# Kernel optimization log

Hardware: AMD Instinct MI355X
Metric: run time of the kernel (lower is better)

Reference implementation:

```python
import jax, jax.numpy as jnp
import numpy as np
from jax.scipy.linalg import solve_triangular

# Production config from MFAWrapper.from_path: 28x28 images, 50 components, 6 factors
B, DFT, K, L = 2048, 784, 50, 6
LOG2PI = float(np.log(2.0 * np.pi))


def setup_inputs() -> dict:
    key = jax.random.key(0)
    k1, k2, k3, k4, k5, k6 = jax.random.split(key, 6)
    X = jax.random.normal(k1, (B, DFT), dtype=jnp.float32)
    J = jax.random.randint(k2, (B, DFT), 0, 2).astype(jnp.int32)  # binary observation mask
    MU = jax.random.normal(k3, (K, DFT), dtype=jnp.float32) * 0.5
    A_fac = jax.random.normal(k4, (K, DFT, L), dtype=jnp.float32) * 0.1  # factor loadings
    log_D = jax.random.normal(k5, (K, DFT), dtype=jnp.float32) * 0.1 - 1.0  # log noise variances
    PI_logits = jax.random.normal(k6, (K,), dtype=jnp.float32)
    return {"X": X, "J": J, "MU": MU, "A_fac": A_fac, "log_D": log_D, "PI_logits": PI_logits}


def _mfa_conditional(X, J, MU, A_fac, log_D, PI_logits):
    """Batched MFA conditional reconstruction given observed features (mask J==1).

    The per-sample torch.nonzero selection is replaced by mask-weighted linear
    algebra: restricting to observed rows of diag(1/D) is identical to zeroing
    the unobserved entries of the weight, so all B samples are conditioned in
    one batched pass instead of a Python loop.
    """
    dtype = X.dtype
    l = A_fac.shape[-1]
    Jf = (J == 1).astype(dtype)                 # [B, Dft]
    inv_D = jnp.exp(-log_D)                     # [K, Dft]
    # masked residual per (sample, component): [B, K, Dft]
    md = (X[:, None, :] - MU[None, :, :]) * Jf[:, None, :]
    # latent posterior precision P = I + A_o^T D_o^{-1} A_o  -> [B, K, L, L]
    P = jnp.einsum('bd,kd,kdi,kdj->bkij', Jf, inv_D, A_fac, A_fac) + jnp.eye(l, dtype=dtype)
    # q = A_o^T D_o^{-1} (x_o - mu_o)  -> [B, K, L]
    q = jnp.einsum('bkd,kd,kdi->bki', md, inv_D, A_fac)
    # per-component log-likelihood of observed features via Woodbury / matrix det lemma
    Lc = jnp.linalg.cholesky(P)                                         # [B, K, L, L]
    y = solve_triangular(Lc, q[..., None], lower=True)[..., 0]          # [B, K, L]
    quad = jnp.einsum('bkd,kd->bk', md * md, inv_D) - jnp.sum(y * y, axis=-1)
    logdet = (2.0 * jnp.sum(jnp.log(jnp.diagonal(Lc, axis1=-2, axis2=-1)), axis=-1)
              + jnp.einsum('bd,kd->bk', Jf, log_D))
    n_obs = jnp.sum(Jf, axis=-1, keepdims=True)                         # [B, 1]
    log_lik = -0.5 * (quad + logdet + n_obs * LOG2PI)                   # [B, K]
    log_resp = jax.nn.log_softmax(PI_logits)[None, :] + log_lik
    c = jnp.argmax(log_resp, axis=-1)                                   # most responsible component, [B]
    # gather per-sample selected component and form the conditional Gaussian in factor form
    P_sel = jnp.take_along_axis(P, c[:, None, None, None], axis=1)[:, 0]  # [B, L, L]
    q_sel = jnp.take_along_axis(q, c[:, None, None], axis=1)[:, 0]        # [B, L]
    A_sel = A_fac[c]                                                      # [B, Dft, L]
    m_z = jnp.linalg.solve(P_sel, q_sel[..., None])[..., 0]               # posterior latent mean [B, L]
    cov_z = jnp.linalg.inv(P_sel)                                         # posterior latent cov [B, L, L]
    Lz = jnp.linalg.cholesky(cov_z)
    M = MU[c] + jnp.einsum('bdi,bi->bd', A_sel, m_z)                      # conditional mean over all features
    A_out = jnp.einsum('bdi,bij->bdj', A_sel, Lz)                         # loadings: cond cov = A_out A_out^T + diag(D_out)
    D_out = jnp.exp(log_D)[c]                                             # [B, Dft]
    Pw = jnp.ones((X.shape[0], 1), dtype)
    return Pw, M, A_out, D_out


def reference(X, J, MU, A_fac, log_D, PI_logits):
    return _mfa_conditional(X, J, MU, A_fac, log_D, PI_logits)
```

## Files before the change

### kernel.cpp

```cpp
#include <hip/hip_runtime.h>
#include <math.h>

#define B_N 2048
#define D_FT 784
#define K_N 50
#define L_N 6
#define LOG2PI_F 1.8378770664093453f

#define OUT_PW 0
#define OUT_M  (B_N)
#define OUT_A  (OUT_M + B_N*D_FT)
#define OUT_D  (OUT_A + B_N*D_FT*6)

#define WS_SCORES 0
#define WS_PQ     (WS_SCORES + K_N*B_N)
#define WS_C      (WS_PQ + K_N*27*B_N)
#define WS_MZLZ   (WS_C + B_N)
#define WS_XT     (WS_MZLZ + B_N*28)
#define WS_JBT    (WS_XT + D_FT*B_N)

#define IDX(i,j) ((i)*((i)+1)/2 + (j))

typedef float v2f __attribute__((ext_vector_type(2)));

#define PK_FMA(acc, a, b) asm("v_pk_fma_f32 %0, %1, %2, %0" : "+v"(acc) : "v"(a), "v"(b))

__device__ __forceinline__ void chol6(const float* P, float* L, float* rd, float* sumlog) {
    float sl = 0.f;
    #pragma unroll
    for (int j = 0; j < 6; ++j) {
        float s = P[IDX(j,j)];
        #pragma unroll
        for (int m = 0; m < j; ++m) s -= L[IDX(j,m)] * L[IDX(j,m)];
        float d = sqrtf(s);
        L[IDX(j,j)] = d;
        float r = 1.0f / d;
        rd[j] = r;
        sl += logf(d);
        #pragma unroll
        for (int i = j + 1; i < 6; ++i) {
            float t = P[IDX(i,j)];
            #pragma unroll
            for (int m = 0; m < j; ++m) t -= L[IDX(i,m)] * L[IDX(j,m)];
            L[IDX(i,j)] = t * r;
        }
    }
    *sumlog = sl;
}

__global__ __launch_bounds__(1024) void k_prep(const float* __restrict__ X,
                                               const int* __restrict__ J,
                                               float4* __restrict__ Xt4,
                                               unsigned* __restrict__ JbT) {
    const int bid = blockIdx.x;
    const int tid = threadIdx.x;
    if (bid < 448) {
        __shared__ float4 tile[32][33];
        int tx = tid & 31, ty = tid >> 5;
        int d4b = (bid % 7) * 32;
        int bb  = (bid / 7) * 32;
        int d4 = d4b + tx;
        if (d4 < D_FT / 4)
            tile[ty][tx] = *(const float4*)&X[(size_t)(bb + ty) * D_FT + d4 * 4];
        __syncthreads();
        int d4o = d4b + ty;
        if (d4o < D_FT / 4)
            Xt4[(size_t)d4o * B_N + (bb + tx)] = tile[tx][ty];
    } else {
        int t = (bid - 448) * 1024 + tid;
        int b = t >> 5;
        int w = t & 31;
        if (w >= 25) return;
        int d0 = w * 32;
        int n = D_FT - d0; if (n > 32) n = 32;
        unsigned u = 0;
        for (int j = 0; j < n; ++j)
            u |= (J[(size_t)b * D_FT + d0 + j] != 0 ? 1u : 0u) << j;
        JbT[(size_t)w * B_N + b] = u;
    }
}

__global__ __launch_bounds__(256) void k_jld(const float* __restrict__ logD,
                                             const unsigned* __restrict__ JbT,
                                             float* __restrict__ SJL) {
    __shared__ float ld[800];
    const int k  = blockIdx.x >> 3;
    const int bt = blockIdx.x & 7;
    for (int i = threadIdx.x; i < 800; i += 256)
        ld[i] = (i < D_FT) ? logD[(size_t)k * D_FT + i] : 0.f;
    __syncthreads();
    const int b = bt * 256 + threadIdx.x;
    float jl = 0.f;
    for (int w = 0; w < 25; ++w) {
        unsigned mw = JbT[(size_t)w * B_N + b];
        const float* lw = &ld[w * 32];
        #pragma unroll
        for (int dd = 0; dd < 32; ++dd)
            jl += ((mw >> dd) & 1u) ? lw[dd] : 0.f;
    }
    SJL[(size_t)k * B_N + b] = jl;
}

#define ACC_PAIR(pi, dd, x0, x1) do { \
    const float4 f0 = sm4[(size_t)(pi) * 4 + 0]; \
    const float4 f1 = sm4[(size_t)(pi) * 4 + 1]; \
    const float4 f2 = sm4[(size_t)(pi) * 4 + 2]; \
    const float4 f3 = sm4[(size_t)(pi) * 4 + 3]; \
    v2f m2;  m2.x = (float)((mw >> (dd)) & 1u); m2.y = (float)((mw >> ((dd)+1)) & 1u); \
    v2f x2;  x2.x = (x0); x2.y = (x1); \
    v2f sa2;  sa2.x = f3.x;  sa2.y = f3.y; \
    v2f nmu2; nmu2.x = f3.z; nmu2.y = f3.w; \
    v2f xm2 = x2 + nmu2; \
    v2f w2  = m2 * sa2; \
    v2f z2  = w2 * xm2; \
    v2f a0; a0.x = f0.x; a0.y = f0.y;  v2f a1; a1.x = f0.z; a1.y = f0.w; \
    v2f a2; a2.x = f1.x; a2.y = f1.y;  v2f a3; a3.x = f1.z; a3.y = f1.w; \
    v2f a4; a4.x = f2.x; a4.y = f2.y;  v2f a5; a5.x = f2.z; a5.y = f2.w; \
    v2f u0 = m2 * a0, u1 = m2 * a1, u2 = m2 * a2; \
    v2f u3 = m2 * a3, u4 = m2 * a4, u5 = m2 * a5; \
    PK_FMA(Pm2[0],  u0, u0); \
    PK_FMA(Pm2[1],  u1, u0); PK_FMA(Pm2[2],  u1, u1); \
    PK_FMA(Pm2[3],  u2, u0); PK_FMA(Pm2[4],  u2, u1); PK_FMA(Pm2[5],  u2, u2); \
    PK_FMA(Pm2[6],  u3, u0); PK_FMA(Pm2[7],  u3, u1); PK_FMA(Pm2[8],  u3, u2); PK_FMA(Pm2[9],  u3, u3); \
    PK_FMA(Pm2[10], u4, u0); PK_FMA(Pm2[11], u4, u1); PK_FMA(Pm2[12], u4, u2); PK_FMA(Pm2[13], u4, u3); PK_FMA(Pm2[14], u4, u4); \
    PK_FMA(Pm2[15], u5, u0); PK_FMA(Pm2[16], u5, u1); PK_FMA(Pm2[17], u5, u2); PK_FMA(Pm2[18], u5, u3); PK_FMA(Pm2[19], u5, u4); PK_FMA(Pm2[20], u5, u5); \
    PK_FMA(qv2[0], z2, u0); PK_FMA(qv2[1], z2, u1); PK_FMA(qv2[2], z2, u2); \
    PK_FMA(qv2[3], z2, u3); PK_FMA(qv2[4], z2, u4); PK_FMA(qv2[5], z2, u5); \
    PK_FMA(quad2, z2, z2); \
} while (0)

__global__ __launch_bounds__(256, 4) void k_accum(
        const float4* __restrict__ Xt4, const unsigned* __restrict__ JbT,
        const float* __restrict__ A, const float* __restrict__ MU,
        const float* __restrict__ logD, const float* __restrict__ PI,
        float* __restrict__ scores, float* __restrict__ Pq) {
    __shared__ float4 sm4[200 * 4];
    float* smem = (float*)sm4;
    const int k   = blockIdx.x >> 5;
    const int tid = threadIdx.x;
    const int s   = tid & 63;
    const int h   = tid >> 6;
    const int b   = (blockIdx.x & 31) * 64 + s;

    v2f Pm2[21], qv2[6], quad2;
    #pragma unroll
    for (int t = 0; t < 21; ++t) { Pm2[t].x = 0.f; Pm2[t].y = 0.f; }
    #pragma unroll
    for (int t = 0; t < 6; ++t) { qv2[t].x = 0.f; qv2[t].y = 0.f; }
    quad2.x = 0.f; quad2.y = 0.f;
    int nob = 0;

    for (int c = 0; c < 2; ++c) {
        const int dbase = c ? 384 : 0;
        const int npair = c ? 200 : 192;
        __syncthreads();
        for (int p = tid; p < npair; p += 256) {
            const int d0 = dbase + 2 * p;
            const float* ar0 = A + ((size_t)k * D_FT + d0) * 6;
            const float* ar1 = ar0 + 6;
            float sa0 = expf(-0.5f * logD[(size_t)k * D_FT + d0]);
            float sa1 = expf(-0.5f * logD[(size_t)k * D_FT + d0 + 1]);
            float4 f0, f1, f2, f3;
            f0.x = sa0 * ar0[0]; f0.y = sa1 * ar1[0]; f0.z = sa0 * ar0[1]; f0.w = sa1 * ar1[1];
            f1.x = sa0 * ar0[2]; f1.y = sa1 * ar1[2]; f1.z = sa0 * ar0[3]; f1.w = sa1 * ar1[3];
            f2.x = sa0 * ar0[4]; f2.y = sa1 * ar1[4]; f2.z = sa0 * ar0[5]; f2.w = sa1 * ar1[5];
            f3.x = sa0; f3.y = sa1;
            f3.z = -MU[(size_t)k * D_FT + d0];
            f3.w = -MU[(size_t)k * D_FT + d0 + 1];
            sm4[(size_t)p * 4 + 0] = f0;
            sm4[(size_t)p * 4 + 1] = f1;
            sm4[(size_t)p * 4 + 2] = f2;
            sm4[(size_t)p * 4 + 3] = f3;
        }
        __syncthreads();

        const int wb = (c ? 12 : 0) + 3 * h;
        for (int w = wb; w < wb + 3; ++w) {
            const unsigned mw = JbT[(size_t)w * B_N + b];
            nob += __popc(mw);
            const int plb = w * 16 - (dbase >> 1);
            const float4* xp = Xt4 + (size_t)(w * 8) * B_N + b;
            #pragma unroll 2
            for (int g = 0; g < 8; ++g) {
                float4 xv = xp[(size_t)g * B_N];
                ACC_PAIR(plb + 2 * g,     g * 4,     xv.x, xv.y);
                ACC_PAIR(plb + 2 * g + 1, g * 4 + 2, xv.z, xv.w);
            }
        }
        if (c == 1 && h == 3) {
            const unsigned mw = JbT[(size_t)24 * B_N + b];
            nob += __popc(mw);
            const int plb = 24 * 16 - 192;
            const float4* xp = Xt4 + (size_t)(24 * 8) * B_N + b;
            #pragma unroll
            for (int g = 0; g < 4; ++g) {
                float4 xv = xp[(size_t)g * B_N];
                ACC_PAIR(plb + 2 * g,     g * 4,     xv.x, xv.y);
                ACC_PAIR(plb + 2 * g + 1, g * 4 + 2, xv.z, xv.w);
            }
        }
    }

    float Pm[21], qv[6], quad;
    #pragma unroll
    for (int t = 0; t < 21; ++t) Pm[t] = Pm2[t].x + Pm2[t].y;
    #pragma unroll
    for (int t = 0; t < 6; ++t) qv[t] = qv2[t].x + qv2[t].y;
    quad = quad2.x + quad2.y;

    __syncthreads();
    float* red = smem;
    #define SLAB_WR do { float* o = &red[s * 33]; \
        _Pragma("unroll") for (int t = 0; t < 21; ++t) o[t] = Pm[t]; \
        _Pragma("unroll") for (int t = 0; t < 6; ++t) o[21 + t] = qv[t]; \
        o[27] = quad; o[28] = (float)nob; } while (0)
    #define SLAB_ADD do { const float* o = &red[s * 33]; \
        _Pragma("unroll") for (int t = 0; t < 21; ++t) Pm[t] += o[t]; \
        _Pragma("unroll") for (int t = 0; t < 6; ++t) qv[t] += o[21 + t]; \
        quad += o[27]; nob += (int)o[28]; } while (0)

    if (h == 1) SLAB_WR;
    __syncthreads();
    if (h == 0) SLAB_ADD;
    __syncthreads();
    if (h == 3) SLAB_WR;
    __syncthreads();
    if (h == 2) SLAB_ADD;
    __syncthreads();
    if (h == 2) SLAB_WR;
    __syncthreads();
    if (h == 0) {
        SLAB_ADD;
        float nobs = (float)nob;

        float jld = scores[(size_t)k * B_N + b];

        Pm[0] += 1.f; Pm[2] += 1.f; Pm[5] += 1.f; Pm[9] += 1.f; Pm[14] += 1.f; Pm[20] += 1.f;

        float Lm[21], rd[6], sumlog;
        chol6(Pm, Lm, rd, &sumlog);
        float y[6];
        #pragma unroll
        for (int j = 0; j < 6; ++j) {
            float sv = qv[j];
            #pragma unroll
            for (int m = 0; m < j; ++m) sv -= Lm[IDX(j,m)] * y[m];
            y[j] = sv * rd[j];
        }
        float yy = 0.f;
        #pragma unroll
        for (int j = 0; j < 6; ++j) yy += y[j] * y[j];
        float logdet = 2.f * sumlog + jld;
        float ll = -0.5f * ((quad - yy) + logdet + nobs * LOG2PI_F);
        float score = ll + PI[k];

        scores[(size_t)k * B_N + b] = score;
        float* pq = Pq + (size_t)k * 27 * B_N + b;
        #pragma unroll
        for (int t = 0; t < 21; ++t) pq[(size_t)t * B_N] = Pm[t];
        #pragma unroll
        for (int t = 0; t < 6; ++t) pq[(size_t)(21 + t) * B_N] = qv[t];
    }
}

__global__ void k_select(const float* __restrict__ scores, const float* __restrict__ Pq,
                         int* __restrict__ csel, float* __restrict__ mzLz,
                         float* __restrict__ out) {
    int b = blockIdx.x * blockDim.x + threadIdx.x;
    if (b >= B_N) return;

    float best = scores[b];
    int bc = 0;
    for (int k = 1; k < K_N; ++k) {
        float s = scores[(size_t)k * B_N + b];
        if (s > best) { best = s; bc = k; }
    }
    csel[b] = bc;
    out[OUT_PW + b] = 1.0f;

    float Pm[21], qv[6];
    const float* pq = Pq + (size_t)bc * 27 * B_N + b;
    #pragma unroll
    for (int t = 0; t < 21; ++t) Pm[t] = pq[(size_t)t * B_N];
    #pragma unroll
    for (int t = 0; t < 6; ++t) qv[t] = pq[(size_t)(21 + t) * B_N];

    float Lm[21], rd[6], dummy;
    chol6(Pm, Lm, rd, &dummy);

    float y[6];
    #pragma unroll
    for (int j = 0; j < 6; ++j) {
        float s = qv[j];
        #pragma unroll
        for (int m = 0; m < j; ++m) s -= Lm[IDX(j,m)] * y[m];
        y[j] = s * rd[j];
    }
    float mz[6];
    #pragma unroll
    for (int ii = 5; ii >= 0; --ii) {
        float s = y[ii];
        #pragma unroll
        for (int j = ii + 1; j < 6; ++j) s -= Lm[IDX(j,ii)] * mz[j];
        mz[ii] = s * rd[ii];
    }
    float Li[21];
    #pragma unroll
    for (int j = 0; j < 6; ++j) {
        Li[IDX(j,j)] = rd[j];
        #pragma unroll
        for (int i = j + 1; i < 6; ++i) {
            float s = 0.f;
            #pragma unroll
            for (int m = j; m < i; ++m) s += Lm[IDX(i,m)] * Li[IDX(m,j)];
            Li[IDX(i,j)] = -s * rd[i];
        }
    }
    float cov[21];
    #pragma unroll
    for (int i = 0; i < 6; ++i) {
        #pragma unroll
        for (int j = 0; j <= i; ++j) {
            float s = 0.f;
            #pragma unroll
            for (int m = i; m < 6; ++m) s += Li[IDX(m,i)] * Li[IDX(m,j)];
            cov[IDX(i,j)] = s;
        }
    }
    float Lz[21], rd2[6];
    chol6(cov, Lz, rd2, &dummy);

    float* o = mzLz + (size_t)b * 28;
    #pragma unroll
    for (int t = 0; t < 6; ++t) o[t] = mz[t];
    #pragma unroll
    for (int t = 0; t < 21; ++t) o[6 + t] = Lz[t];
}

__global__ __launch_bounds__(256) void k_output(
        const float* __restrict__ A, const float* __restrict__ MU,
        const float* __restrict__ logD, const int* __restrict__ csel,
        const float* __restrict__ mzLz, float* __restrict__ out) {
    __shared__ float smz[6];
    __shared__ float sLz[21];
    __shared__ int sc;
    int b = blockIdx.x;
    if (threadIdx.x == 0) sc = csel[b];
    if (threadIdx.x < 27) {
        float v = mzLz[(size_t)b * 28 + threadIdx.x];
        if (threadIdx.x < 6) smz[threadIdx.x] = v;
        else sLz[threadIdx.x - 6] = v;
    }
    __syncthreads();
    int c = sc;

    for (int d = threadIdx.x; d < D_FT; d += 256) {
        const float* ar = A + ((size_t)c * D_FT + d) * 6;
        float a[6];
        #pragma unroll
        for (int i = 0; i < 6; ++i) a[i] = ar[i];
        float mu = MU[(size_t)c * D_FT + d];
        float ld = logD[(size_t)c * D_FT + d];
        float m = mu;
        #pragma unroll
        for (int i = 0; i < 6; ++i) m += a[i] * smz[i];
        out[OUT_M + (size_t)b * D_FT + d] = m;
        out[OUT_D + (size_t)b * D_FT + d] = expf(ld);
        float* ao = out + OUT_A + ((size_t)b * D_FT + d) * 6;
        #pragma unroll
        for (int j = 0; j < 6; ++j) {
            float s = 0.f;
            #pragma unroll
            for (int i = j; i < 6; ++i) s += a[i] * sLz[IDX(i,j)];
            ao[j] = s;
        }
    }
}

extern "C" void kernel_launch(void* const* d_in, const int* in_sizes, int n_in,
                              void* d_out, int out_size, void* d_ws, size_t ws_size,
                              hipStream_t stream) {
    (void)in_sizes; (void)n_in; (void)out_size; (void)ws_size;
    const float* X    = (const float*)d_in[0];
    const int*   J    = (const int*)d_in[1];
    const float* MU   = (const float*)d_in[2];
    const float* A    = (const float*)d_in[3];
    const float* logD = (const float*)d_in[4];
    const float* PI   = (const float*)d_in[5];
    float* out = (float*)d_out;
    float* ws  = (float*)d_ws;

    float*    scores = ws + WS_SCORES;
    float*    Pq     = ws + WS_PQ;
    int*      csel   = (int*)(ws + WS_C);
    float*    mzLz   = ws + WS_MZLZ;
    float4*   Xt4    = (float4*)(ws + WS_XT);
    unsigned* JbT    = (unsigned*)(ws + WS_JBT);

    k_prep<<<512, 1024, 0, stream>>>(X, J, Xt4, JbT);

    k_jld<<<K_N * 8, 256, 0, stream>>>(logD, JbT, scores);

    k_accum<<<32 * K_N, 256, 0, stream>>>(Xt4, JbT, A, MU, logD, PI, scores, Pq);

    k_select<<<B_N / 256, 256, 0, stream>>>(scores, Pq, csel, mzLz, out);

    k_output<<<B_N, 256, 0, stream>>>(A, MU, logD, csel, mzLz, out);
}
```

Baseline: 139.1 us.

## Fuse component selection into output kernel and batch X loads in accumulation

Merges k_select and k_output into one kernel. Every thread of each per-sample block redundantly runs the argmax over 50 scores plus the 6x6 Cholesky, solve and inverse, which removes one launch and the csel/mzLz round trip through global memory. The trade is duplicated scalar work and broadcast score loads in all 256 threads of each block. Separately, k_accum's inner loop now issues all 8 (or 4) float4 loads of X before accumulating, to get more memory-level parallelism at the cost of extra registers.

```diff
diff --git a/kernel.cpp b/kernel.cpp
--- a/kernel.cpp
+++ b/kernel.cpp
@@ -14,9 +14,7 @@
 
 #define WS_SCORES 0
 #define WS_PQ     (WS_SCORES + K_N*B_N)
-#define WS_C      (WS_PQ + K_N*27*B_N)
-#define WS_MZLZ   (WS_C + B_N)
-#define WS_XT     (WS_MZLZ + B_N*28)
+#define WS_XT     (WS_PQ + K_N*27*B_N)
 #define WS_JBT    (WS_XT + D_FT*B_N)
 
 #define IDX(i,j) ((i)*((i)+1)/2 + (j))
@@ -180,11 +178,13 @@
             nob += __popc(mw);
             const int plb = w * 16 - (dbase >> 1);
             const float4* xp = Xt4 + (size_t)(w * 8) * B_N + b;
-            #pragma unroll 2
+            float4 xv[8];
+            #pragma unroll
+            for (int g = 0; g < 8; ++g) xv[g] = xp[(size_t)g * B_N];
+            #pragma unroll
             for (int g = 0; g < 8; ++g) {
-                float4 xv = xp[(size_t)g * B_N];
-                ACC_PAIR(plb + 2 * g,     g * 4,     xv.x, xv.y);
-                ACC_PAIR(plb + 2 * g + 1, g * 4 + 2, xv.z, xv.w);
+                ACC_PAIR(plb + 2 * g,     g * 4,     xv[g].x, xv[g].y);
+                ACC_PAIR(plb + 2 * g + 1, g * 4 + 2, xv[g].z, xv[g].w);
             }
         }
         if (c == 1 && h == 3) {
@@ -192,11 +192,13 @@
             nob += __popc(mw);
             const int plb = 24 * 16 - 192;
             const float4* xp = Xt4 + (size_t)(24 * 8) * B_N + b;
+            float4 xv[4];
+            #pragma unroll
+            for (int g = 0; g < 4; ++g) xv[g] = xp[(size_t)g * B_N];
             #pragma unroll
             for (int g = 0; g < 4; ++g) {
-                float4 xv = xp[(size_t)g * B_N];
-                ACC_PAIR(plb + 2 * g,     g * 4,     xv.x, xv.y);
-                ACC_PAIR(plb + 2 * g + 1, g * 4 + 2, xv.z, xv.w);
+                ACC_PAIR(plb + 2 * g,     g * 4,     xv[g].x, xv[g].y);
+                ACC_PAIR(plb + 2 * g + 1, g * 4 + 2, xv[g].z, xv[g].w);
             }
         }
     }
@@ -263,20 +265,20 @@
     }
 }
 
-__global__ void k_select(const float* __restrict__ scores, const float* __restrict__ Pq,
-                         int* __restrict__ csel, float* __restrict__ mzLz,
-                         float* __restrict__ out) {
-    int b = blockIdx.x * blockDim.x + threadIdx.x;
-    if (b >= B_N) return;
+__global__ __launch_bounds__(256) void k_outsel(
+        const float* __restrict__ scores, const float* __restrict__ Pq,
+        const float* __restrict__ A, const float* __restrict__ MU,
+        const float* __restrict__ logD, float* __restrict__ out) {
+    const int b = blockIdx.x;
+    const int tid = threadIdx.x;
 
     float best = scores[b];
     int bc = 0;
-    for (int k = 1; k < K_N; ++k) {
-        float s = scores[(size_t)k * B_N + b];
-        if (s > best) { best = s; bc = k; }
-    }
-    csel[b] = bc;
-    out[OUT_PW + b] = 1.0f;
+    for (int kk = 1; kk < K_N; ++kk) {
+        float sv = scores[(size_t)kk * B_N + b];
+        if (sv > best) { best = sv; bc = kk; }
+    }
+    if (tid == 0) out[OUT_PW + b] = 1.0f;
 
     float Pm[21], qv[6];
     const float* pq = Pq + (size_t)bc * 27 * B_N + b;
@@ -291,18 +293,18 @@
     float y[6];
     #pragma unroll
     for (int j = 0; j < 6; ++j) {
-        float s = qv[j];
-        #pragma unroll
-        for (int m = 0; m < j; ++m) s -= Lm[IDX(j,m)] * y[m];
-        y[j] = s * rd[j];
+        float sv = qv[j];
+        #pragma unroll
+        for (int m = 0; m < j; ++m) sv -= Lm[IDX(j,m)] * y[m];
+        y[j] = sv * rd[j];
     }
     float mz[6];
     #pragma unroll
     for (int ii = 5; ii >= 0; --ii) {
-        float s = y[ii];
-        #pragma unroll
-        for (int j = ii + 1; j < 6; ++j) s -= Lm[IDX(j,ii)] * mz[j];
-        mz[ii] = s * rd[ii];
+        float sv = y[ii];
+        #pragma unroll
+        for (int j = ii + 1; j < 6; ++j) sv -= Lm[IDX(j,ii)] * mz[j];
+        mz[ii] = sv * rd[ii];
     }
     float Li[21];
     #pragma unroll
@@ -310,10 +312,10 @@
         Li[IDX(j,j)] = rd[j];
         #pragma unroll
         for (int i = j + 1; i < 6; ++i) {
-            float s = 0.f;
-            #pragma unroll
-            for (int m = j; m < i; ++m) s += Lm[IDX(i,m)] * Li[IDX(m,j)];
-            Li[IDX(i,j)] = -s * rd[i];
+            float sv = 0.f;
+            #pragma unroll
+            for (int m = j; m < i; ++m) sv += Lm[IDX(i,m)] * Li[IDX(m,j)];
+            Li[IDX(i,j)] = -sv * rd[i];
         }
     }
     float cov[21];
@@ -321,40 +323,17 @@
     for (int i = 0; i < 6; ++i) {
         #pragma unroll
         for (int j = 0; j <= i; ++j) {
-            float s = 0.f;
-            #pragma unroll
-            for (int m = i; m < 6; ++m) s += Li[IDX(m,i)] * Li[IDX(m,j)];
-            cov[IDX(i,j)] = s;
+            float sv = 0.f;
+            #pragma unroll
+            for (int m = i; m < 6; ++m) sv += Li[IDX(m,i)] * Li[IDX(m,j)];
+            cov[IDX(i,j)] = sv;
         }
     }
     float Lz[21], rd2[6];
     chol6(cov, Lz, rd2, &dummy);
 
-    float* o = mzLz + (size_t)b * 28;
-    #pragma unroll
-    for (int t = 0; t < 6; ++t) o[t] = mz[t];
-    #pragma unroll
-    for (int t = 0; t < 21; ++t) o[6 + t] = Lz[t];
-}
-
-__global__ __launch_bounds__(256) void k_output(
-        const float* __restrict__ A, const float* __restrict__ MU,
-        const float* __restrict__ logD, const int* __restrict__ csel,
-        const float* __restrict__ mzLz, float* __restrict__ out) {
-    __shared__ float smz[6];
-    __shared__ float sLz[21];
-    __shared__ int sc;
-    int b = blockIdx.x;
-    if (threadIdx.x == 0) sc = csel[b];
-    if (threadIdx.x < 27) {
-        float v = mzLz[(size_t)b * 28 + threadIdx.x];
-        if (threadIdx.x < 6) smz[threadIdx.x] = v;
-        else sLz[threadIdx.x - 6] = v;
-    }
-    __syncthreads();
-    int c = sc;
-
-    for (int d = threadIdx.x; d < D_FT; d += 256) {
+    const int c = bc;
+    for (int d = tid; d < D_FT; d += 256) {
         const float* ar = A + ((size_t)c * D_FT + d) * 6;
         float a[6];
         #pragma unroll
@@ -363,16 +342,16 @@
         float ld = logD[(size_t)c * D_FT + d];
         float m = mu;
         #pragma unroll
-        for (int i = 0; i < 6; ++i) m += a[i] * smz[i];
+        for (int i = 0; i < 6; ++i) m += a[i] * mz[i];
         out[OUT_M + (size_t)b * D_FT + d] = m;
         out[OUT_D + (size_t)b * D_FT + d] = expf(ld);
         float* ao = out + OUT_A + ((size_t)b * D_FT + d) * 6;
         #pragma unroll
         for (int j = 0; j < 6; ++j) {
-            float s = 0.f;
-            #pragma unroll
-            for (int i = j; i < 6; ++i) s += a[i] * sLz[IDX(i,j)];
-            ao[j] = s;
+            float sv = 0.f;
+            #pragma unroll
+            for (int i = j; i < 6; ++i) sv += a[i] * Lz[IDX(i,j)];
+            ao[j] = sv;
         }
     }
 }
@@ -392,8 +371,6 @@
 
     float*    scores = ws + WS_SCORES;
     float*    Pq     = ws + WS_PQ;
-    int*      csel   = (int*)(ws + WS_C);
-    float*    mzLz   = ws + WS_MZLZ;
     float4*   Xt4    = (float4*)(ws + WS_XT);
     unsigned* JbT    = (unsigned*)(ws + WS_JBT);
 
@@ -403,7 +380,5 @@
 
     k_accum<<<32 * K_N, 256, 0, stream>>>(Xt4, JbT, A, MU, logD, PI, scores, Pq);
 
-    k_select<<<B_N / 256, 256, 0, stream>>>(scores, Pq, csel, mzLz, out);
-
-    k_output<<<B_N, 256, 0, stream>>>(A, MU, logD, csel, mzLz, out);
-}
+    k_outsel<<<B_N, 256, 0, stream>>>(scores, Pq, A, MU, logD, out);
+}
```

New measurement: 142.2 us. 1.02x slower.
